# Optimization experiments

Measured on AMD Instinct MI355X. Metric: run time of the kernel, lower is better.

Reference implementation:

```python
import jax, jax.numpy as jnp
import numpy as np

N, E, D = 100000, 1600000, 128      # nodes, edges, in_channels = MLP out_dim
L = 3                               # num GIN layers
OC = D + L * D                      # concat width = 512
CH, CHID = 4, 256                   # num ChannelMLPs, their hidden dim


def setup_inputs() -> dict:
    key = jax.random.key(0)
    ks = jax.random.split(key, 10)
    s = lambda fan_in: 1.0 / np.sqrt(fan_in)
    x = jax.random.normal(ks[0], (N, D), dtype=jnp.float32)
    edge_index = jax.random.randint(ks[1], (2, E), 0, N, dtype=jnp.int32)
    # conv MLPs: per layer 3 linear layers (in->hid, hid->hid, hid->out), all 128x128
    convW = jax.random.normal(ks[2], (L, 3, D, D), dtype=jnp.float32) * s(D)
    convB = jnp.zeros((L, 3, D), dtype=jnp.float32)
    # channel MLPs: 512 -> 256 -> 256 -> 1, ReLU after every layer (output_activation='relu')
    chanW1 = jax.random.normal(ks[3], (CH, OC, CHID), dtype=jnp.float32) * s(OC)
    chanB1 = jnp.zeros((CH, CHID), dtype=jnp.float32)
    chanW2 = jax.random.normal(ks[4], (CH, CHID, CHID), dtype=jnp.float32) * s(CHID)
    chanB2 = jnp.zeros((CH, CHID), dtype=jnp.float32)
    chanW3 = jax.random.normal(ks[5], (CH, CHID, 1), dtype=jnp.float32) * s(CHID)
    chanB3 = jnp.zeros((CH, 1), dtype=jnp.float32)
    return {"x": x, "edge_index": edge_index, "convW": convW, "convB": convB,
            "chanW1": chanW1, "chanB1": chanB1, "chanW2": chanW2, "chanB2": chanB2,
            "chanW3": chanW3, "chanB3": chanB3}


def reference(x, edge_index, convW, convB, chanW1, chanB1, chanW2, chanB2, chanW3, chanB3):
    src, dst = edge_index[0], edge_index[1]
    n = x.shape[0]
    feats = [x]                      # skip_first_features=False -> keep input
    h = x
    for l in range(L):
        # GINConv, eps=0: mlp((1+eps)*h + sum_{j in N(i)} h_j)
        agg = jax.ops.segment_sum(h[src], dst, num_segments=n)  # scatter-add at targets
        h = h + agg
        for k in range(3):           # MLP: Lin+ReLU x3 (2 hidden + relu output activation)
            h = jax.nn.relu(h @ convW[l, k] + convB[l, k])
        feats.append(h)
    xcat = jnp.concatenate(feats, axis=1)                       # [N, 512]
    # channel MLPs vectorized over the channel axis c
    h1 = jax.nn.relu(jnp.einsum('nd,cdh->cnh', xcat, chanW1) + chanB1[:, None, :])
    h2 = jax.nn.relu(jnp.einsum('cnh,chk->cnk', h1, chanW2) + chanB2[:, None, :])
    h3 = jax.nn.relu(jnp.einsum('cnh,cho->cno', h2, chanW3) + chanB3[:, None, :])
    return jnp.transpose(h3[..., 0])                            # [N, num_ChannelMLPs]
```

## Files before the change

kernel.cpp:

```cpp
#include <hip/hip_runtime.h>
#include <hip/hip_bf16.h>

#define D 128
#define NLAYER 3
#define NCH 4

typedef __attribute__((ext_vector_type(8))) short short8;
typedef __attribute__((ext_vector_type(4))) float f32x4;

__device__ __forceinline__ ushort f2bf(float f) {
    unsigned int u = __builtin_bit_cast(unsigned int, f);
    u += 0x7fffu + ((u >> 16) & 1u);
    return (ushort)(u >> 16);
}
__device__ __forceinline__ float bflo(unsigned int u) {
    return __builtin_bit_cast(float, u << 16);
}
__device__ __forceinline__ float bfhi(unsigned int u) {
    return __builtin_bit_cast(float, u & 0xffff0000u);
}

#define FILL_CHUNK 4096
__global__ __launch_bounds__(256) void hist_part_kernel(
    const int* __restrict__ dst, int* __restrict__ deg,
    int E, int nPer, int N)
{
    int cls = blockIdx.x & 7;
    int base = (blockIdx.x >> 3) * FILL_CHUNK;
    int lo = cls * nPer;
    int hi = lo + nPer; if (hi > N) hi = N;
    int end = base + FILL_CHUNK; if (end > E) end = E;
    for (int e = base + threadIdx.x; e < end; e += 256) {
        int d = dst[e];
        if (d >= lo && d < hi) atomicAdd(&deg[d], 1);
    }
}

__global__ __launch_bounds__(256) void blocksum_kernel(
    const int* __restrict__ deg, int* __restrict__ bsum, int n)
{
    int i = blockIdx.x * 256 + threadIdx.x;
    int v = (i < n) ? deg[i] : 0;
#pragma unroll
    for (int o = 1; o < 64; o <<= 1) v += __shfl_xor(v, o);
    __shared__ int s[4];
    if ((threadIdx.x & 63) == 0) s[threadIdx.x >> 6] = v;
    __syncthreads();
    if (threadIdx.x == 0) bsum[blockIdx.x] = s[0] + s[1] + s[2] + s[3];
}

__global__ __launch_bounds__(512) void scanblk_kernel(
    const int* __restrict__ bsum, int* __restrict__ boff, int nb,
    int* __restrict__ offs, int n, int E)
{
    __shared__ int sh[512];
    int t = threadIdx.x;
    sh[t] = (t < nb) ? bsum[t] : 0;
    __syncthreads();
    for (int d = 1; d < 512; d <<= 1) {
        int v = (t >= d) ? sh[t - d] : 0;
        __syncthreads();
        sh[t] += v;
        __syncthreads();
    }
    if (t < nb) boff[t] = (t == 0) ? 0 : sh[t - 1];
    if (t == 0) offs[n] = E;
}

__global__ __launch_bounds__(256) void blockscan_kernel(
    const int* __restrict__ deg, const int* __restrict__ boff,
    int* __restrict__ offs, int* __restrict__ cursor, int n)
{
    __shared__ int sh[256];
    int t = threadIdx.x;
    int i = blockIdx.x * 256 + t;
    int v = (i < n) ? deg[i] : 0;
    sh[t] = v;
    __syncthreads();
    for (int d = 1; d < 256; d <<= 1) {
        int u = (t >= d) ? sh[t - d] : 0;
        __syncthreads();
        sh[t] += u;
        __syncthreads();
    }
    if (i < n) {
        int ex = boff[blockIdx.x] + sh[t] - v;
        offs[i] = ex; cursor[i] = ex;
    }
}

__global__ __launch_bounds__(256) void fill_part_kernel(
    const int* __restrict__ src, const int* __restrict__ dst,
    int* __restrict__ cursor, int* __restrict__ csr,
    int E, int nPer, int N)
{
    int cls = blockIdx.x & 7;
    int base = (blockIdx.x >> 3) * FILL_CHUNK;
    int lo = cls * nPer;
    int hi = lo + nPer; if (hi > N) hi = N;
    int end = base + FILL_CHUNK; if (end > E) end = E;
    for (int e = base + threadIdx.x; e < end; e += 256) {
        int d = dst[e];
        int s = src[e];
        if (d >= lo && d < hi) {
            int p = atomicAdd(&cursor[d], 1);
            csr[p] = s;
        }
    }
}

__global__ __launch_bounds__(256) void cvtx_kernel(
    const float* __restrict__ x, ushort* __restrict__ xb, int total8)
{
    int i = blockIdx.x * 256 + threadIdx.x;
    if (i >= total8) return;
    const float* gp = x + (size_t)i * 8;
    float4 v0 = *(const float4*)gp;
    float4 v1 = *(const float4*)(gp + 4);
    short8 pk;
    pk[0] = (short)f2bf(v0.x); pk[1] = (short)f2bf(v0.y);
    pk[2] = (short)f2bf(v0.z); pk[3] = (short)f2bf(v0.w);
    pk[4] = (short)f2bf(v1.x); pk[5] = (short)f2bf(v1.y);
    pk[6] = (short)f2bf(v1.z); pk[7] = (short)f2bf(v1.w);
    *(short8*)(xb + (size_t)i * 8) = pk;
}

__global__ void cvtW_kernel(const float* __restrict__ W, ushort* __restrict__ Wt,
                            int K, int Ncols) {
    __shared__ float tile[32][33];
    int c = blockIdx.z;
    int k0 = blockIdx.x * 32, n0 = blockIdx.y * 32;
    const float* Wc = W + (size_t)c * K * Ncols;
    ushort* Wtc = Wt + (size_t)c * K * Ncols;
    int tx = threadIdx.x & 31, ty = threadIdx.x >> 5;
#pragma unroll
    for (int i = 0; i < 4; ++i) {
        int k = k0 + ty + i * 8;
        tile[ty + i * 8][tx] = Wc[(size_t)k * Ncols + n0 + tx];
    }
    __syncthreads();
#pragma unroll
    for (int i = 0; i < 4; ++i) {
        int n = n0 + ty + i * 8;
        Wtc[(size_t)n * K + k0 + tx] = f2bf(tile[tx][ty + i * 8]);
    }
}

__global__ __launch_bounds__(256) void agg_bf16(
    const ushort* __restrict__ h,
    const int* __restrict__ offs, const int* __restrict__ csr,
    ushort* __restrict__ outb, int n)
{
    int node = (blockIdx.x * 256 + threadIdx.x) >> 4;
    int l16 = threadIdx.x & 15;
    if (node >= n) return;
    const uint4* hb = (const uint4*)h;
    uint4 u = hb[(size_t)node * 16 + l16 >> 0];
    u = *((const uint4*)(h + (size_t)node * 128) + l16);
    float a0 = bflo(u.x), a1 = bfhi(u.x);
    float a2 = bflo(u.y), a3 = bfhi(u.y);
    float a4 = bflo(u.z), a5 = bfhi(u.z);
    float a6 = bflo(u.w), a7 = bfhi(u.w);
    int b = offs[node], e = offs[node + 1];
    int j = b;
    for (; j + 4 <= e; j += 4) {
        int s0 = csr[j], s1 = csr[j + 1], s2 = csr[j + 2], s3 = csr[j + 3];
        uint4 v0 = *((const uint4*)(h + (size_t)s0 * 128) + l16);
        uint4 v1 = *((const uint4*)(h + (size_t)s1 * 128) + l16);
        uint4 v2 = *((const uint4*)(h + (size_t)s2 * 128) + l16);
        uint4 v3 = *((const uint4*)(h + (size_t)s3 * 128) + l16);
        a0 += (bflo(v0.x) + bflo(v1.x)) + (bflo(v2.x) + bflo(v3.x));
        a1 += (bfhi(v0.x) + bfhi(v1.x)) + (bfhi(v2.x) + bfhi(v3.x));
        a2 += (bflo(v0.y) + bflo(v1.y)) + (bflo(v2.y) + bflo(v3.y));
        a3 += (bfhi(v0.y) + bfhi(v1.y)) + (bfhi(v2.y) + bfhi(v3.y));
        a4 += (bflo(v0.z) + bflo(v1.z)) + (bflo(v2.z) + bflo(v3.z));
        a5 += (bfhi(v0.z) + bfhi(v1.z)) + (bfhi(v2.z) + bfhi(v3.z));
        a6 += (bflo(v0.w) + bflo(v1.w)) + (bflo(v2.w) + bflo(v3.w));
        a7 += (bfhi(v0.w) + bfhi(v1.w)) + (bfhi(v2.w) + bfhi(v3.w));
    }
    for (; j < e; ++j) {
        uint4 v0 = *((const uint4*)(h + (size_t)csr[j] * 128) + l16);
        a0 += bflo(v0.x); a1 += bfhi(v0.x);
        a2 += bflo(v0.y); a3 += bfhi(v0.y);
        a4 += bflo(v0.z); a5 += bfhi(v0.z);
        a6 += bflo(v0.w); a7 += bfhi(v0.w);
    }
    uint4 po;
    po.x = (unsigned int)f2bf(a0) | ((unsigned int)f2bf(a1) << 16);
    po.y = (unsigned int)f2bf(a2) | ((unsigned int)f2bf(a3) << 16);
    po.z = (unsigned int)f2bf(a4) | ((unsigned int)f2bf(a5) << 16);
    po.w = (unsigned int)f2bf(a6) | ((unsigned int)f2bf(a7) << 16);
    *((uint4*)(outb + (size_t)node * 128) + l16) = po;
}

__global__ __launch_bounds__(256) void gin_mlp_mfma(
    const ushort* __restrict__ A,
    const ushort* __restrict__ WtL,
    const float* __restrict__ biasL,
    ushort* __restrict__ Out,
    int nrows)
{
    __shared__ __align__(16) ushort As[128 * 128];
    __shared__ __align__(16) ushort Bs[128 * 128];
    const int t = threadIdx.x;
    const int w = t >> 6, lane = t & 63;
    const int quad = lane >> 4, c15 = lane & 15;
    const int wr = w >> 1, wc = w & 1;
    const int rowbase = blockIdx.x * 128;

#pragma unroll
    for (int i = 0; i < 8; ++i) {
        int lin = (i * 4 + w) * 64 + lane;
        int row = lin >> 4, slot = lin & 15, g = slot ^ (row & 15);
        int grow = rowbase + row;
        if (grow >= nrows) grow = 0;
        const ushort* gp = A + (size_t)grow * 128 + g * 8;
        __builtin_amdgcn_global_load_lds(
            (const __attribute__((address_space(1))) void*)gp,
            (__attribute__((address_space(3))) void*)&As[(i * 4 + w) * 512],
            16, 0, 0);
    }
#pragma unroll
    for (int i = 0; i < 8; ++i) {
        int lin = (i * 4 + w) * 64 + lane;
        int n = lin >> 4, slot = lin & 15, g = slot ^ (n & 15);
        const ushort* gp = WtL + (size_t)n * 128 + g * 8;
        __builtin_amdgcn_global_load_lds(
            (const __attribute__((address_space(1))) void*)gp,
            (__attribute__((address_space(3))) void*)&Bs[(i * 4 + w) * 512],
            16, 0, 0);
    }
    __syncthreads();

    for (int s = 0; s < 3; ++s) {
        f32x4 acc[4][4];
#pragma unroll
        for (int i = 0; i < 4; ++i)
#pragma unroll
            for (int j = 0; j < 4; ++j)
#pragma unroll
                for (int r = 0; r < 4; ++r) acc[i][j][r] = 0.f;

#pragma unroll
        for (int ks = 0; ks < 4; ++ks) {
            short8 af[4], bf[4];
#pragma unroll
            for (int tr = 0; tr < 4; ++tr) {
                int r = wr * 64 + tr * 16 + c15;
                af[tr] = *(const short8*)&As[r * 128 + (((ks * 4 + quad) ^ (r & 15)) * 8)];
            }
#pragma unroll
            for (int tc = 0; tc < 4; ++tc) {
                int n = wc * 64 + tc * 16 + c15;
                bf[tc] = *(const short8*)&Bs[n * 128 + (((ks * 4 + quad) ^ (n & 15)) * 8)];
            }
#pragma unroll
            for (int tr = 0; tr < 4; ++tr)
#pragma unroll
                for (int tc = 0; tc < 4; ++tc)
                    acc[tr][tc] = __builtin_amdgcn_mfma_f32_16x16x32_bf16(
                        af[tr], bf[tc], acc[tr][tc], 0, 0, 0);
        }
        __syncthreads();

        if (s < 2) {
#pragma unroll
            for (int tc = 0; tc < 4; ++tc) {
                int col = wc * 64 + tc * 16 + c15;
                float bv = biasL[s * 128 + col];
#pragma unroll
                for (int tr = 0; tr < 4; ++tr)
#pragma unroll
                    for (int rg = 0; rg < 4; ++rg) {
                        int row = wr * 64 + tr * 16 + quad * 4 + rg;
                        As[row * 128 + (((col >> 3) ^ (row & 15)) * 8) + (col & 7)]
                            = f2bf(fmaxf(acc[tr][tc][rg] + bv, 0.f));
                    }
            }
            const ushort* Wn = WtL + (size_t)(s + 1) * 128 * 128;
#pragma unroll
            for (int i = 0; i < 8; ++i) {
                int lin = (i * 4 + w) * 64 + lane;
                int n = lin >> 4, slot = lin & 15, g = slot ^ (n & 15);
                const ushort* gp = Wn + (size_t)n * 128 + g * 8;
                __builtin_amdgcn_global_load_lds(
                    (const __attribute__((address_space(1))) void*)gp,
                    (__attribute__((address_space(3))) void*)&Bs[(i * 4 + w) * 512],
                    16, 0, 0);
            }
            __syncthreads();
        } else {
#pragma unroll
            for (int tc = 0; tc < 4; ++tc) {
                int col = wc * 64 + tc * 16 + c15;
                float bv = biasL[2 * 128 + col];
#pragma unroll
                for (int tr = 0; tr < 4; ++tr)
#pragma unroll
                    for (int rg = 0; rg < 4; ++rg) {
                        int grow = rowbase + wr * 64 + tr * 16 + quad * 4 + rg;
                        if (grow < nrows)
                            Out[(size_t)grow * 128 + col]
                                = f2bf(fmaxf(acc[tr][tc][rg] + bv, 0.f));
                    }
            }
        }
    }
}

__global__ __launch_bounds__(256, 2) void chan_fused_mfma(
    const ushort* __restrict__ A0, const ushort* __restrict__ A1,
    const ushort* __restrict__ A2, const ushort* __restrict__ A3,
    const ushort* __restrict__ Wt1,
    const float* __restrict__ b1,
    const ushort* __restrict__ Wt2,
    const float* __restrict__ b2,
    const float* __restrict__ w3,
    const float* __restrict__ b3,
    float* __restrict__ out,
    int N, int T, int chunkT)
{
    const int bid = blockIdx.x;
    const int xcd = bid & 7;
    const int idx = bid >> 3;
    const int c = idx & 3;
    const int rt = xcd * chunkT + (idx >> 2);
    if (rt >= T) return;
    const int rowbase = rt * 64;

    __shared__ __align__(16) ushort As[64 * 64];
    __shared__ __align__(16) ushort Bs[256 * 64];
    __shared__ __align__(16) ushort Ts[64 * 256];
    __shared__ float red[64][4];
    const int t = threadIdx.x;
    const int w = t >> 6, lane = t & 63;
    const int quad = lane >> 4, c15 = lane & 15;
    const ushort* Asrc[4] = {A0, A1, A2, A3};
    const ushort* W1c = Wt1 + (size_t)c * 256 * 512;
    const ushort* W2c = Wt2 + (size_t)c * 256 * 256;

    f32x4 acc[4][4];
#pragma unroll
    for (int i = 0; i < 4; ++i)
#pragma unroll
        for (int j = 0; j < 4; ++j)
#pragma unroll
            for (int r = 0; r < 4; ++r) acc[i][j][r] = 0.f;

    for (int kc = 0; kc < 512; kc += 64) {
        const ushort* Ab = Asrc[kc >> 7];
        const int within = kc & 127;
#pragma unroll
        for (int i = 0; i < 2; ++i) {
            int lin = (i * 4 + w) * 64 + lane;
            int row = lin >> 3, slot = lin & 7, g = slot ^ (row & 7);
            int grow = rowbase + row;
            if (grow >= N) grow = 0;
            const ushort* gp = Ab + (size_t)grow * 128 + within + g * 8;
            __builtin_amdgcn_global_load_lds(
                (const __attribute__((address_space(1))) void*)gp,
                (__attribute__((address_space(3))) void*)&As[(i * 4 + w) * 512],
                16, 0, 0);
        }
#pragma unroll
        for (int i = 0; i < 8; ++i) {
            int lin = (i * 4 + w) * 64 + lane;
            int n = lin >> 3, slot = lin & 7, g = slot ^ (n & 7);
            const ushort* gp = W1c + (size_t)n * 512 + kc + g * 8;
            __builtin_amdgcn_global_load_lds(
                (const __attribute__((address_space(1))) void*)gp,
                (__attribute__((address_space(3))) void*)&Bs[(i * 4 + w) * 512],
                16, 0, 0);
        }
        __syncthreads();
#pragma unroll
        for (int ks = 0; ks < 2; ++ks) {
            const int K8 = ks * 4;
            short8 af[4], bf[4];
#pragma unroll
            for (int tr = 0; tr < 4; ++tr) {
                int r = tr * 16 + c15;
                af[tr] = *(const short8*)&As[r * 64 + (((K8 + quad) ^ (r & 7)) * 8)];
            }
#pragma unroll
            for (int tc = 0; tc < 4; ++tc) {
                int n = w * 64 + tc * 16 + c15;
                bf[tc] = *(const short8*)&Bs[n * 64 + (((K8 + quad) ^ (n & 7)) * 8)];
            }
#pragma unroll
            for (int tr = 0; tr < 4; ++tr)
#pragma unroll
                for (int tc = 0; tc < 4; ++tc)
                    acc[tr][tc] = __builtin_amdgcn_mfma_f32_16x16x32_bf16(
                        af[tr], bf[tc], acc[tr][tc], 0, 0, 0);
        }
        __syncthreads();
    }

#pragma unroll
    for (int tc = 0; tc < 4; ++tc) {
        int col = w * 64 + tc * 16 + c15;
        float bv = b1[c * 256 + col];
#pragma unroll
        for (int tr = 0; tr < 4; ++tr)
#pragma unroll
            for (int rg = 0; rg < 4; ++rg) {
                int row = tr * 16 + quad * 4 + rg;
                Ts[row * 256 + (((col >> 3) ^ (row & 31)) * 8) + (col & 7)]
                    = f2bf(fmaxf(acc[tr][tc][rg] + bv, 0.f));
            }
    }
    __syncthreads();

#pragma unroll
    for (int i = 0; i < 4; ++i)
#pragma unroll
        for (int j = 0; j < 4; ++j)
#pragma unroll
            for (int r = 0; r < 4; ++r) acc[i][j][r] = 0.f;

    for (int kc = 0; kc < 256; kc += 64) {
#pragma unroll
        for (int i = 0; i < 8; ++i) {
            int lin = (i * 4 + w) * 64 + lane;
            int n = lin >> 3, slot = lin & 7, g = slot ^ (n & 7);
            const ushort* gp = W2c + (size_t)n * 256 + kc + g * 8;
            __builtin_amdgcn_global_load_lds(
                (const __attribute__((address_space(1))) void*)gp,
                (__attribute__((address_space(3))) void*)&Bs[(i * 4 + w) * 512],
                16, 0, 0);
        }
        __syncthreads();
#pragma unroll
        for (int ks = 0; ks < 2; ++ks) {
            short8 af[4], bf[4];
            const int g0 = (kc >> 3) + ks * 4 + quad;
#pragma unroll
            for (int tr = 0; tr < 4; ++tr) {
                int r = tr * 16 + c15;
                af[tr] = *(const short8*)&Ts[r * 256 + ((g0 ^ (r & 31)) * 8)];
            }
#pragma unroll
            for (int tc = 0; tc < 4; ++tc) {
                int n = w * 64 + tc * 16 + c15;
                bf[tc] = *(const short8*)&Bs[n * 64 + ((((ks * 4) + quad) ^ (n & 7)) * 8)];
            }
#pragma unroll
            for (int tr = 0; tr < 4; ++tr)
#pragma unroll
                for (int tc = 0; tc < 4; ++tc)
                    acc[tr][tc] = __builtin_amdgcn_mfma_f32_16x16x32_bf16(
                        af[tr], bf[tc], acc[tr][tc], 0, 0, 0);
        }
        __syncthreads();
    }

    float b2v[4], w3v[4];
#pragma unroll
    for (int tc = 0; tc < 4; ++tc) {
        int col = w * 64 + tc * 16 + c15;
        b2v[tc] = b2[c * 256 + col];
        w3v[tc] = w3[c * 256 + col];
    }
#pragma unroll
    for (int tr = 0; tr < 4; ++tr)
#pragma unroll
        for (int rg = 0; rg < 4; ++rg) {
            float p = 0.f;
#pragma unroll
            for (int tc = 0; tc < 4; ++tc)
                p += fmaxf(acc[tr][tc][rg] + b2v[tc], 0.f) * w3v[tc];
            p += __shfl_xor(p, 1);
            p += __shfl_xor(p, 2);
            p += __shfl_xor(p, 4);
            p += __shfl_xor(p, 8);
            if (c15 == 0) red[tr * 16 + quad * 4 + rg][w] = p;
        }
    __syncthreads();
    if (t < 64) {
        int grow = rowbase + t;
        if (grow < N) {
            float s = red[t][0] + red[t][1] + red[t][2] + red[t][3] + b3[c];
            out[(size_t)grow * NCH + c] = fmaxf(s, 0.f);
        }
    }
}

extern "C" void kernel_launch(void* const* d_in, const int* in_sizes, int n_in,
                              void* d_out, int out_size, void* d_ws, size_t ws_size,
                              hipStream_t stream) {
    const float* x        = (const float*)d_in[0];
    const int*   eidx     = (const int*)d_in[1];
    const float* convW    = (const float*)d_in[2];
    const float* convB    = (const float*)d_in[3];
    const float* chanW1   = (const float*)d_in[4];
    const float* chanB1   = (const float*)d_in[5];
    const float* chanW2   = (const float*)d_in[6];
    const float* chanB2   = (const float*)d_in[7];
    const float* chanW3   = (const float*)d_in[8];
    const float* chanB3   = (const float*)d_in[9];
    float* out = (float*)d_out;

    const int N = in_sizes[0] / D;
    const int E = in_sizes[1] / 2;
    const int* srcp = eidx;
    const int* dstp = eidx + E;
    const int nb = (N + 255) / 256;

    char* w = (char*)d_ws;
    auto take = [&](size_t bytes) {
        char* p = w;
        w += (bytes + 255) & ~(size_t)255;
        return p;
    };
    ushort* xb     = (ushort*)take((size_t)N * D * 2);
    ushort* h0     = (ushort*)take((size_t)N * D * 2);
    ushort* h1     = (ushort*)take((size_t)N * D * 2);
    ushort* h2     = (ushort*)take((size_t)N * D * 2);
    int*    deg    = (int*)take((size_t)N * 4);
    int*    offs   = (int*)take((size_t)(N + 1) * 4);
    int*    cursor = (int*)take((size_t)N * 4);
    int*    bsum   = (int*)take((size_t)nb * 4);
    int*    boff   = (int*)take((size_t)nb * 4);
    ushort* Wt1b   = (ushort*)take((size_t)NCH * 256 * 512 * 2);
    ushort* Wt2b   = (ushort*)take((size_t)NCH * 256 * 256 * 2);
    ushort* WtC    = (ushort*)take((size_t)NLAYER * 3 * D * D * 2);

    size_t used = (size_t)(w - (char*)d_ws);
    if (used > ws_size) return;
    size_t rem = ws_size - used;
    size_t need_gin = (((size_t)E * 4 + 255) & ~(size_t)255) + (size_t)N * D * 2;
    if (rem < need_gin) return;

    int*    csr = (int*)w;
    ushort* a   = (ushort*)(w + (((size_t)E * 4 + 255) & ~(size_t)255));

    hipMemsetAsync(deg, 0, (size_t)N * 4, stream);
    {
        int nchunks = (E + FILL_CHUNK - 1) / FILL_CHUNK;
        int nPer = (N + 7) / 8;
        hist_part_kernel<<<nchunks * 8, 256, 0, stream>>>(dstp, deg, E, nPer, N);
        blocksum_kernel<<<nb, 256, 0, stream>>>(deg, bsum, N);
        scanblk_kernel<<<1, 512, 0, stream>>>(bsum, boff, nb, offs, N, E);
        blockscan_kernel<<<nb, 256, 0, stream>>>(deg, boff, offs, cursor, N);
        fill_part_kernel<<<nchunks * 8, 256, 0, stream>>>(
            srcp, dstp, cursor, csr, E, nPer, N);
    }

    cvtx_kernel<<<(N * 16 + 255) / 256, 256, 0, stream>>>(x, xb, N * 16);
    cvtW_kernel<<<dim3(512 / 32, 256 / 32, NCH), 256, 0, stream>>>(chanW1, Wt1b, 512, 256);
    cvtW_kernel<<<dim3(256 / 32, 256 / 32, NCH), 256, 0, stream>>>(chanW2, Wt2b, 256, 256);
    cvtW_kernel<<<dim3(D / 32, D / 32, NLAYER * 3), 256, 0, stream>>>(convW, WtC, D, D);

    const int rowtiles = (N + 127) / 128;
    const int aggblocks = (N * 16 + 255) / 256;

    ushort* hbuf[NLAYER] = {h0, h1, h2};
    const ushort* prev = xb;
    for (int l = 0; l < NLAYER; ++l) {
        agg_bf16<<<aggblocks, 256, 0, stream>>>(prev, offs, csr, a, N);
        gin_mlp_mfma<<<rowtiles, 256, 0, stream>>>(
            a, WtC + (size_t)l * 3 * D * D, convB + (size_t)l * 3 * D, hbuf[l], N);
        prev = hbuf[l];
    }

    {
        const int T = (N + 63) / 64;
        const int chunkT = (T + 7) / 8;
        const int grid = 8 * chunkT * NCH;
        chan_fused_mfma<<<grid, 256, 0, stream>>>(
            xb, h0, h1, h2,
            Wt1b, chanB1, Wt2b, chanB2, chanW3, chanB3,
            out, N, T, chunkT);
    }
}
```

Baseline: 832.0 us.

## Double-buffer channel MLP GEMM LDS tiles with K=32 stages and prefetch

Replaces the single-buffered K=64 LDS tiles in the fused channel-MLP kernel with two K=32 buffers. The next stage's global-to-LDS loads are issued before the current stage's MFMAs, and the first W2 tile is prefetched during the last W1 stage, so load latency overlaps compute and one barrier per stage is removed. It also changes the XOR swizzle to fit 32-wide rows and cleans up a redundant load in the aggregation kernel. The cost is twice as many loop iterations with smaller MFMA batches, and correctness now depends on the new swizzle and buffer indexing being right.

```diff
diff --git a/kernel.cpp b/kernel.cpp
--- a/kernel.cpp
+++ b/kernel.cpp
@@ -154,9 +154,7 @@
     int node = (blockIdx.x * 256 + threadIdx.x) >> 4;
     int l16 = threadIdx.x & 15;
     if (node >= n) return;
-    const uint4* hb = (const uint4*)h;
-    uint4 u = hb[(size_t)node * 16 + l16 >> 0];
-    u = *((const uint4*)(h + (size_t)node * 128) + l16);
+    uint4 u = *((const uint4*)(h + (size_t)node * 128) + l16);
     float a0 = bflo(u.x), a1 = bfhi(u.x);
     float a2 = bflo(u.y), a3 = bfhi(u.y);
     float a4 = bflo(u.z), a5 = bfhi(u.z);
@@ -328,72 +326,85 @@
     if (rt >= T) return;
     const int rowbase = rt * 64;
 
-    __shared__ __align__(16) ushort As[64 * 64];
-    __shared__ __align__(16) ushort Bs[256 * 64];
+    __shared__ __align__(16) ushort As2[2][64 * 32];
+    __shared__ __align__(16) ushort Bs2[2][256 * 32];
     __shared__ __align__(16) ushort Ts[64 * 256];
     __shared__ float red[64][4];
     const int t = threadIdx.x;
     const int w = t >> 6, lane = t & 63;
     const int quad = lane >> 4, c15 = lane & 15;
-    const ushort* Asrc[4] = {A0, A1, A2, A3};
     const ushort* W1c = Wt1 + (size_t)c * 256 * 512;
     const ushort* W2c = Wt2 + (size_t)c * 256 * 256;
 
-    f32x4 acc[4][4];
-#pragma unroll
-    for (int i = 0; i < 4; ++i)
-#pragma unroll
-        for (int j = 0; j < 4; ++j)
-#pragma unroll
-            for (int r = 0; r < 4; ++r) acc[i][j][r] = 0.f;
-
-    for (int kc = 0; kc < 512; kc += 64) {
-        const ushort* Ab = Asrc[kc >> 7];
-        const int within = kc & 127;
-#pragma unroll
-        for (int i = 0; i < 2; ++i) {
-            int lin = (i * 4 + w) * 64 + lane;
-            int row = lin >> 3, slot = lin & 7, g = slot ^ (row & 7);
-            int grow = rowbase + row;
-            if (grow >= N) grow = 0;
-            const ushort* gp = Ab + (size_t)grow * 128 + within + g * 8;
+    const int a_lin = w * 64 + lane;
+    const int a_row = a_lin >> 2, a_slot = a_lin & 3;
+    const int a_g = a_slot ^ ((a_row >> 1) & 3);
+    int a_grow = rowbase + a_row; if (a_grow >= N) a_grow = 0;
+    int b_n[4], b_g[4];
+#pragma unroll
+    for (int i = 0; i < 4; ++i) {
+        int lin = (i * 4 + w) * 64 + lane;
+        b_n[i] = lin >> 2;
+        b_g[i] = (lin & 3) ^ ((b_n[i] >> 1) & 3);
+    }
+
+    auto stageA = [&](int buf, int kc) {
+        int ai = kc >> 7;
+        const ushort* Ab = (ai == 0) ? A0 : (ai == 1) ? A1 : (ai == 2) ? A2 : A3;
+        const ushort* gp = Ab + (size_t)a_grow * 128 + (kc & 127) + a_g * 8;
+        __builtin_amdgcn_global_load_lds(
+            (const __attribute__((address_space(1))) void*)gp,
+            (__attribute__((address_space(3))) void*)&As2[buf][w * 512],
+            16, 0, 0);
+    };
+    auto stageB = [&](int buf, const ushort* Wn, int ldk, int kc) {
+#pragma unroll
+        for (int i = 0; i < 4; ++i) {
+            const ushort* gp = Wn + (size_t)b_n[i] * ldk + kc + b_g[i] * 8;
             __builtin_amdgcn_global_load_lds(
                 (const __attribute__((address_space(1))) void*)gp,
-                (__attribute__((address_space(3))) void*)&As[(i * 4 + w) * 512],
+                (__attribute__((address_space(3))) void*)&Bs2[buf][(i * 4 + w) * 512],
                 16, 0, 0);
         }
-#pragma unroll
-        for (int i = 0; i < 8; ++i) {
-            int lin = (i * 4 + w) * 64 + lane;
-            int n = lin >> 3, slot = lin & 7, g = slot ^ (n & 7);
-            const ushort* gp = W1c + (size_t)n * 512 + kc + g * 8;
-            __builtin_amdgcn_global_load_lds(
-                (const __attribute__((address_space(1))) void*)gp,
-                (__attribute__((address_space(3))) void*)&Bs[(i * 4 + w) * 512],
-                16, 0, 0);
-        }
-        __syncthreads();
-#pragma unroll
-        for (int ks = 0; ks < 2; ++ks) {
-            const int K8 = ks * 4;
-            short8 af[4], bf[4];
-#pragma unroll
-            for (int tr = 0; tr < 4; ++tr) {
-                int r = tr * 16 + c15;
-                af[tr] = *(const short8*)&As[r * 64 + (((K8 + quad) ^ (r & 7)) * 8)];
-            }
-#pragma unroll
-            for (int tc = 0; tc < 4; ++tc) {
-                int n = w * 64 + tc * 16 + c15;
-                bf[tc] = *(const short8*)&Bs[n * 64 + (((K8 + quad) ^ (n & 7)) * 8)];
-            }
-#pragma unroll
-            for (int tr = 0; tr < 4; ++tr)
-#pragma unroll
-                for (int tc = 0; tc < 4; ++tc)
-                    acc[tr][tc] = __builtin_amdgcn_mfma_f32_16x16x32_bf16(
-                        af[tr], bf[tc], acc[tr][tc], 0, 0, 0);
-        }
+    };
+
+    f32x4 acc[4][4];
+#pragma unroll
+    for (int i = 0; i < 4; ++i)
+#pragma unroll
+        for (int j = 0; j < 4; ++j)
+#pragma unroll
+            for (int r = 0; r < 4; ++r) acc[i][j][r] = 0.f;
+
+    stageA(0, 0);
+    stageB(0, W1c, 512, 0);
+    __syncthreads();
+#pragma unroll 2
+    for (int s = 0; s < 16; ++s) {
+        const int cur = s & 1, nxt = cur ^ 1;
+        if (s < 15) {
+            stageA(nxt, (s + 1) * 32);
+            stageB(nxt, W1c, 512, (s + 1) * 32);
+        } else {
+            stageB(nxt, W2c, 256, 0);
+        }
+        short8 af[4], bf[4];
+#pragma unroll
+        for (int tr = 0; tr < 4; ++tr) {
+            int r = tr * 16 + c15;
+            af[tr] = *(const short8*)&As2[cur][r * 32 + ((quad ^ ((r >> 1) & 3)) * 8)];
+        }
+#pragma unroll
+        for (int tc = 0; tc < 4; ++tc) {
+            int n = w * 64 + tc * 16 + c15;
+            bf[tc] = *(const short8*)&Bs2[cur][n * 32 + ((quad ^ ((n >> 1) & 3)) * 8)];
+        }
+#pragma unroll
+        for (int tr = 0; tr < 4; ++tr)
+#pragma unroll
+            for (int tc = 0; tc < 4; ++tc)
+                acc[tr][tc] = __builtin_amdgcn_mfma_f32_16x16x32_bf16(
+                    af[tr], bf[tc], acc[tr][tc], 0, 0, 0);
         __syncthreads();
     }
 
@@ -419,39 +430,28 @@
 #pragma unroll
             for (int r = 0; r < 4; ++r) acc[i][j][r] = 0.f;
 
-    for (int kc = 0; kc < 256; kc += 64) {
-#pragma unroll
-        for (int i = 0; i < 8; ++i) {
-            int lin = (i * 4 + w) * 64 + lane;
-            int n = lin >> 3, slot = lin & 7, g = slot ^ (n & 7);
-            const ushort* gp = W2c + (size_t)n * 256 + kc + g * 8;
-            __builtin_amdgcn_global_load_lds(
-                (const __attribute__((address_space(1))) void*)gp,
-                (__attribute__((address_space(3))) void*)&Bs[(i * 4 + w) * 512],
-                16, 0, 0);
-        }
-        __syncthreads();
-#pragma unroll
-        for (int ks = 0; ks < 2; ++ks) {
-            short8 af[4], bf[4];
-            const int g0 = (kc >> 3) + ks * 4 + quad;
-#pragma unroll
-            for (int tr = 0; tr < 4; ++tr) {
-                int r = tr * 16 + c15;
-                af[tr] = *(const short8*)&Ts[r * 256 + ((g0 ^ (r & 31)) * 8)];
-            }
-#pragma unroll
-            for (int tc = 0; tc < 4; ++tc) {
-                int n = w * 64 + tc * 16 + c15;
-                bf[tc] = *(const short8*)&Bs[n * 64 + ((((ks * 4) + quad) ^ (n & 7)) * 8)];
-            }
-#pragma unroll
-            for (int tr = 0; tr < 4; ++tr)
-#pragma unroll
-                for (int tc = 0; tc < 4; ++tc)
-                    acc[tr][tc] = __builtin_amdgcn_mfma_f32_16x16x32_bf16(
-                        af[tr], bf[tc], acc[tr][tc], 0, 0, 0);
-        }
+#pragma unroll 2
+    for (int s = 0; s < 8; ++s) {
+        const int cur = s & 1, nxt = cur ^ 1;
+        if (s < 7) stageB(nxt, W2c, 256, (s + 1) * 32);
+        short8 af[4], bf[4];
+        const int g0 = s * 4 + quad;
+#pragma unroll
+        for (int tr = 0; tr < 4; ++tr) {
+            int r = tr * 16 + c15;
+            af[tr] = *(const short8*)&Ts[r * 256 + ((g0 ^ (r & 31)) * 8)];
+        }
+#pragma unroll
+        for (int tc = 0; tc < 4; ++tc) {
+            int n = w * 64 + tc * 16 + c15;
+            bf[tc] = *(const short8*)&Bs2[cur][n * 32 + ((quad ^ ((n >> 1) & 3)) * 8)];
+        }
+#pragma unroll
+        for (int tr = 0; tr < 4; ++tr)
+#pragma unroll
+            for (int tc = 0; tc < 4; ++tc)
+                acc[tr][tc] = __builtin_amdgcn_mfma_f32_16x16x32_bf16(
+                    af[tr], bf[tc], acc[tr][tc], 0, 0, 0);
         __syncthreads();
     }
 
```

Result: slower. 885.6 us (+6.4%).
